# Kernel optimization log

Measured on AMD Instinct MI355X. Metric: run time of the kernel, lower is better.

Reference implementation:

```python
import jax, jax.numpy as jnp
import numpy as np

N = 8192
IN_F = 512
OUT_F = 256


def setup_inputs() -> dict:
    key = jax.random.key(0)
    k_x, k_adj, k_w, k_phi = jax.random.split(key, 4)
    x = jax.random.normal(k_x, (N, IN_F), dtype=jnp.float32)
    adj = jax.random.randint(k_adj, (N, N), 0, 2, dtype=jnp.int32)
    stdv_w = 1.0 / np.sqrt(OUT_F)
    weight = jax.random.uniform(k_w, (IN_F, OUT_F), minval=-stdv_w, maxval=stdv_w, dtype=jnp.float32)
    bias = jnp.zeros((OUT_F,), dtype=jnp.float32)
    stdv_p = 1.0  # 1/sqrt(phi.size(1)) = 1/sqrt(1)
    phi = jax.random.uniform(k_phi, (2 * OUT_F, 1), minval=-stdv_p, maxval=stdv_p, dtype=jnp.float32)
    return {"x": x, "adj": adj, "weight": weight, "bias": bias, "phi": phi}


def reference(x, adj, weight, bias, phi):
    # H = X W + b                                   [N, F]
    H = jnp.matmul(x, weight) + bias
    F_out = weight.shape[1]
    # Additive attention score: S[i,j] = [H_i ; H_j] . phi = H_i.phi_src + H_j.phi_dst
    # (H_interleaved indexes rows i, H_expanded indexes cols j in the torch code)
    s_src = jnp.matmul(H, phi[:F_out, 0])           # [N]
    s_dst = jnp.matmul(H, phi[F_out:, 0])           # [N]
    S = s_src[:, None] + s_dst[None, :]             # [N, N]
    n = x.shape[0]
    mask = (adj.astype(jnp.float32) + jnp.eye(n, dtype=jnp.float32)) != 0
    S_masked = jnp.where(mask, S, -jnp.inf)
    A = jax.nn.softmax(S_masked, axis=1)            # [N, N]
    return jnp.matmul(A, H)                         # [N, F]
```

## Files before the change

### kernel.cpp

```cpp
#include <hip/hip_runtime.h>
#include <hip/hip_bf16.h>
#include <stdint.h>

#define N_NODES 8192
#define IN_F 512
#define OUT_F 256
#define KSPLIT 4

typedef __attribute__((ext_vector_type(8))) short bf16x8;
typedef __attribute__((ext_vector_type(4))) float f32x4;

__device__ __forceinline__ unsigned short f2bf_rn(float f) {
  union { float f; unsigned u; } v; v.f = f;
  unsigned r = v.u + 0x7FFFu + ((v.u >> 16) & 1u);
  return (unsigned short)(r >> 16);
}
__device__ __forceinline__ float bf2f(unsigned short h) {
  union { unsigned u; float f; } v; v.u = ((unsigned)h) << 16;
  return v.f;
}

__device__ __forceinline__ void gload_lds16(const void* g, void* l) {
  __builtin_amdgcn_global_load_lds(
      (const __attribute__((address_space(1))) unsigned int*)g,
      (__attribute__((address_space(3))) unsigned int*)l, 16, 0, 0);
}

__device__ __forceinline__ bf16x8 expand8(uint2 b) {
  unsigned c0 = b.x, c1 = b.x >> 16, c2 = b.y, c3 = b.y >> 16;
  uint4 q;
  q.x = ((c0 & 1u) | ((c0 & 0x100u) << 8)) * 0x3F80u;
  q.y = ((c1 & 1u) | ((c1 & 0x100u) << 8)) * 0x3F80u;
  q.z = ((c2 & 1u) | ((c2 & 0x100u) << 8)) * 0x3F80u;
  q.w = ((c3 & 1u) | ((c3 & 0x100u) << 8)) * 0x3F80u;
  union { uint4 u; bf16x8 v; } r; r.u = q;
  return r.v;
}

__global__ __launch_bounds__(256) void k0_prep_w(const float* __restrict__ W,
                                                 short* __restrict__ Wh,
                                                 short* __restrict__ Wl) {
  int k = blockIdx.x;
  int c = threadIdx.x;
  float v = W[(size_t)k * OUT_F + c];
  unsigned short h = f2bf_rn(v);
  unsigned short l = f2bf_rn(v - bf2f(h));
  Wh[(size_t)c * IN_F + k] = (short)h;
  Wl[(size_t)c * IN_F + k] = (short)l;
}

__global__ __launch_bounds__(256) void k1_gemm_h(
    const float* __restrict__ X, const short* __restrict__ Wh,
    const short* __restrict__ Wl, const float* __restrict__ bias,
    float* __restrict__ H) {
  __shared__ __align__(16) short Xh[64 * 64], Xl[64 * 64];
  __shared__ __align__(16) short Wsh[128 * 64], Wsl[128 * 64];
  const int tid = threadIdx.x;
  const int rb = blockIdx.x >> 1, cb = blockIdx.x & 1;
  const int r0 = rb * 64, c0 = cb * 128;
  const int lane = tid & 63, wid = tid >> 6;

  f32x4 acc[8];
#pragma unroll
  for (int i = 0; i < 8; ++i) acc[i] = (f32x4){0.f, 0.f, 0.f, 0.f};

  const int sr = tid >> 2;
  const int sk = (tid & 3) * 16;

  for (int kc = 0; kc < IN_F; kc += 64) {
    const float* xp = X + (size_t)(r0 + sr) * IN_F + kc + sk;
#pragma unroll
    for (int q = 0; q < 2; ++q) {
      f32x4 v0 = *(const f32x4*)(xp + q * 8);
      f32x4 v1 = *(const f32x4*)(xp + q * 8 + 4);
      bf16x8 hv, lv;
#pragma unroll
      for (int j = 0; j < 4; ++j) {
        unsigned short h0 = f2bf_rn(v0[j]);
        hv[j] = (short)h0; lv[j] = (short)f2bf_rn(v0[j] - bf2f(h0));
        unsigned short h1 = f2bf_rn(v1[j]);
        hv[4 + j] = (short)h1; lv[4 + j] = (short)f2bf_rn(v1[j] - bf2f(h1));
      }
      int kb = (sk >> 3) + q;
      int off = sr * 64 + ((kb ^ (sr & 7)) << 3);
      *(bf16x8*)(Xh + off) = hv;
      *(bf16x8*)(Xl + off) = lv;
    }
#pragma unroll
    for (int it = 0; it < 4; ++it) {
      int u = it * 256 + tid;
      int col = u >> 3, kb = u & 7;
      size_t goff = (size_t)(c0 + col) * IN_F + kc + kb * 8;
      int off = col * 64 + ((kb ^ (col & 7)) << 3);
      *(bf16x8*)(Wsh + off) = *(const bf16x8*)(Wh + goff);
      *(bf16x8*)(Wsl + off) = *(const bf16x8*)(Wl + goff);
    }
    __syncthreads();
    const int arow = wid * 16 + (lane & 15);
    const int khalf = lane >> 4;
#pragma unroll
    for (int ks = 0; ks < 2; ++ks) {
      int kb = ks * 4 + khalf;
      int aoff = arow * 64 + ((kb ^ (arow & 7)) << 3);
      bf16x8 ah = *(const bf16x8*)(Xh + aoff);
      bf16x8 al = *(const bf16x8*)(Xl + aoff);
#pragma unroll
      for (int n = 0; n < 8; ++n) {
        int col = n * 16 + (lane & 15);
        int boff = col * 64 + ((kb ^ (col & 7)) << 3);
        bf16x8 bh = *(const bf16x8*)(Wsh + boff);
        bf16x8 bl = *(const bf16x8*)(Wsl + boff);
        acc[n] = __builtin_amdgcn_mfma_f32_16x16x32_bf16(ah, bh, acc[n], 0, 0, 0);
        acc[n] = __builtin_amdgcn_mfma_f32_16x16x32_bf16(ah, bl, acc[n], 0, 0, 0);
        acc[n] = __builtin_amdgcn_mfma_f32_16x16x32_bf16(al, bh, acc[n], 0, 0, 0);
      }
    }
    __syncthreads();
  }
  const int orow = r0 + wid * 16 + ((lane >> 4) << 2);
#pragma unroll
  for (int n = 0; n < 8; ++n) {
    int col = c0 + n * 16 + (lane & 15);
    float b = bias[col];
#pragma unroll
    for (int r = 0; r < 4; ++r)
      H[(size_t)(orow + r) * OUT_F + col] = acc[n][r] + b;
  }
}

__global__ __launch_bounds__(256) void k2_sdst(const float* __restrict__ H,
                                               const float* __restrict__ phi,
                                               float* __restrict__ sdst,
                                               float* __restrict__ blockmax) {
  __shared__ float r4[4];
  const int tid = threadIdx.x, lane = tid & 63, wid = tid >> 6;
  const int row = blockIdx.x * 4 + wid;
  f32x4 hv = *(const f32x4*)(H + (size_t)row * OUT_F + lane * 4);
  f32x4 pv = *(const f32x4*)(phi + OUT_F + lane * 4);
  float s = hv[0] * pv[0] + hv[1] * pv[1] + hv[2] * pv[2] + hv[3] * pv[3];
#pragma unroll
  for (int off = 32; off; off >>= 1) s += __shfl_xor(s, off);
  if (lane == 0) { sdst[row] = s; r4[wid] = s; }
  __syncthreads();
  if (tid == 0)
    blockmax[blockIdx.x] = fmaxf(fmaxf(r4[0], r4[1]), fmaxf(r4[2], r4[3]));
}

__global__ __launch_bounds__(256) void k4_build(const float* __restrict__ H,
                                                const float* __restrict__ sdst,
                                                const float* __restrict__ blockmax,
                                                short* __restrict__ Bs,
                                                float* __restrict__ e) {
  __shared__ float t[64][65];
  __shared__ float red[4];
  const int tid = threadIdx.x;
  float m = -1e30f;
  for (int i = tid; i < 2048; i += 256) m = fmaxf(m, blockmax[i]);
#pragma unroll
  for (int off = 32; off; off >>= 1) m = fmaxf(m, __shfl_xor(m, off));
  if ((tid & 63) == 0) red[tid >> 6] = m;
  __syncthreads();
  const float gmax = fmaxf(fmaxf(red[0], red[1]), fmaxf(red[2], red[3]));

  const int tx = tid & 63, ty = tid >> 6;
  const int j0 = (blockIdx.x >> 2) * 64;
  const int c0 = (blockIdx.x & 3) * 64;
#pragma unroll
  for (int i = 0; i < 16; ++i)
    t[ty + i * 4][tx] = H[(size_t)(j0 + ty + i * 4) * OUT_F + c0 + tx];
  __syncthreads();
  const float ej = expf(sdst[j0 + tx] - gmax);
#pragma unroll
  for (int i = 0; i < 16; ++i) {
    int c = c0 + ty + i * 4;
    float v = ej * t[tx][ty + i * 4];
    unsigned short h = f2bf_rn(v);
    unsigned short l = f2bf_rn(v - bf2f(h));
    size_t kidx = (size_t)j0 + (tx ^ ((c & 7) << 3));
    Bs[(size_t)c * N_NODES + kidx] = (short)h;
    Bs[(size_t)(256 + c) * N_NODES + kidx] = (short)l;
  }
  if (c0 == 0 && tid < 64) e[j0 + tid] = expf(sdst[j0 + tid] - gmax);
}

__global__ __launch_bounds__(512) void k5_main(
    const int* __restrict__ adj, const short* __restrict__ Bs,
    const float* __restrict__ e, float* __restrict__ part,
    float* __restrict__ dpartg, int kchunk) {
  __shared__ __align__(16) unsigned char Ab[2][128 * 64];
  __shared__ __align__(16) short Bb[2][2 * 256 * 64];

  const int tid = threadIdx.x;
  const int bid = (int)(blockIdx.x & 7) * 32 + (int)(blockIdx.x >> 3);
  const int rb = bid & 63, ksi = bid >> 6;
  const int r0 = rb * 128;
  const long kbeg = (long)ksi * kchunk;
  const int lane = tid & 63, wid = tid >> 6;
  const int wr = wid >> 2, wc = wid & 3;

  f32x4 acc[4][4];
#pragma unroll
  for (int mi = 0; mi < 4; ++mi)
#pragma unroll
    for (int ni = 0; ni < 4; ++ni) acc[mi][ni] = (f32x4){0.f, 0.f, 0.f, 0.f};

  const int sr = tid >> 2;
  const int skq = tid & 3;
  const int sk = skq * 16;
  const int irow = r0 + sr;
  float dsum = 0.f;

  int4 a0, a1, a2, a3;
  f32x4 ev0, ev1, ev2, ev3;

  auto issueA = [&](long kc) {
    const int* ap = adj + (size_t)irow * N_NODES + kc + sk;
    a0 = ((const int4*)ap)[0]; a1 = ((const int4*)ap)[1];
    a2 = ((const int4*)ap)[2]; a3 = ((const int4*)ap)[3];
    const float* ep = e + kc + sk;
    ev0 = ((const f32x4*)ep)[0]; ev1 = ((const f32x4*)ep)[1];
    ev2 = ((const f32x4*)ep)[2]; ev3 = ((const f32x4*)ep)[3];
  };
  auto issueB = [&](long kc, int buf) {
    const int p = wid >> 2;
    const int cg = wid & 3;
    const short* base = Bs + (size_t)p * 256 * N_NODES + kc;
#pragma unroll
    for (int i = 0; i < 8; ++i) {
      int col = cg * 64 + i * 8 + (lane >> 3);
      const short* g = base + (size_t)col * N_NODES + (lane & 7) * 8;
      short* l = &Bb[buf][(p * 256 + cg * 64 + i * 8) * 64];
      gload_lds16(g, l);
    }
  };
  auto finishA = [&](int buf) {
    dsum += (float)a0.x * ev0[0] + (float)a0.y * ev0[1] +
            (float)a0.z * ev0[2] + (float)a0.w * ev0[3];
    dsum += (float)a1.x * ev1[0] + (float)a1.y * ev1[1] +
            (float)a1.z * ev1[2] + (float)a1.w * ev1[3];
    dsum += (float)a2.x * ev2[0] + (float)a2.y * ev2[1] +
            (float)a2.z * ev2[2] + (float)a2.w * ev2[3];
    dsum += (float)a3.x * ev3[0] + (float)a3.y * ev3[1] +
            (float)a3.z * ev3[2] + (float)a3.w * ev3[3];
    unsigned u0 = (unsigned)a0.x | ((unsigned)a0.y << 8) |
                  ((unsigned)a0.z << 16) | ((unsigned)a0.w << 24);
    unsigned u1 = (unsigned)a1.x | ((unsigned)a1.y << 8) |
                  ((unsigned)a1.z << 16) | ((unsigned)a1.w << 24);
    unsigned u2 = (unsigned)a2.x | ((unsigned)a2.y << 8) |
                  ((unsigned)a2.z << 16) | ((unsigned)a2.w << 24);
    unsigned u3 = (unsigned)a3.x | ((unsigned)a3.y << 8) |
                  ((unsigned)a3.z << 16) | ((unsigned)a3.w << 24);
    const int g0 = skq * 2, g1 = g0 + 1;
    uint2 w0; w0.x = u0; w0.y = u1;
    uint2 w1; w1.x = u2; w1.y = u3;
    *(uint2*)&Ab[buf][sr * 64 + ((g0 ^ (sr & 7)) << 3)] = w0;
    *(uint2*)&Ab[buf][sr * 64 + ((g1 ^ (sr & 7)) << 3)] = w1;
  };
  auto compute = [&](int buf) {
#pragma unroll
    for (int ks = 0; ks < 2; ++ks) {
      const int kb = ks * 4 + (lane >> 4);
      bf16x8 af[4];
#pragma unroll
      for (int mi = 0; mi < 4; ++mi) {
        int row = wr * 64 + mi * 16 + (lane & 15);
        uint2 b = *(const uint2*)&Ab[buf][row * 64 + ((kb ^ (row & 7)) << 3)];
        af[mi] = expand8(b);
      }
#pragma unroll
      for (int ni = 0; ni < 4; ++ni) {
        int col = wc * 64 + ni * 16 + (lane & 15);
        int so = (kb ^ (col & 7)) << 3;
        bf16x8 bh = *(const bf16x8*)&Bb[buf][col * 64 + so];
        bf16x8 bl = *(const bf16x8*)&Bb[buf][(256 + col) * 64 + so];
#pragma unroll
        for (int mi = 0; mi < 4; ++mi) {
          acc[mi][ni] = __builtin_amdgcn_mfma_f32_16x16x32_bf16(af[mi], bh, acc[mi][ni], 0, 0, 0);
          acc[mi][ni] = __builtin_amdgcn_mfma_f32_16x16x32_bf16(af[mi], bl, acc[mi][ni], 0, 0, 0);
        }
      }
    }
  };

  issueA(kbeg); issueB(kbeg, 0); finishA(0);
  __syncthreads();

  const int NT = kchunk >> 6;
  for (int t = 0; t < NT; ++t) {
    const int cur = t & 1;
    if (t + 1 < NT) {
      const long kc = kbeg + (long)(t + 1) * 64;
      issueA(kc);
      issueB(kc, cur ^ 1);
    }
    compute(cur);
    if (t + 1 < NT) finishA(cur ^ 1);
    __syncthreads();
  }

  dsum += __shfl_xor(dsum, 1);
  dsum += __shfl_xor(dsum, 2);
  if ((tid & 3) == 0) dpartg[(size_t)ksi * N_NODES + irow] = dsum;

  float* pbase = part + (size_t)ksi * N_NODES * OUT_F;
  const int orow0 = r0 + wr * 64 + ((lane >> 4) << 2);
#pragma unroll
  for (int mi = 0; mi < 4; ++mi) {
    int orow = orow0 + mi * 16;
#pragma unroll
    for (int ni = 0; ni < 4; ++ni) {
      int col = wc * 64 + ni * 16 + (lane & 15);
#pragma unroll
      for (int r = 0; r < 4; ++r)
        pbase[(size_t)(orow + r) * OUT_F + col] = acc[mi][ni][r];
    }
  }
}

__global__ __launch_bounds__(256) void k6_final(const float* __restrict__ part,
                                                const float* __restrict__ dpart,
                                                const float* __restrict__ H,
                                                const float* __restrict__ e,
                                                const int* __restrict__ adj,
                                                float* __restrict__ out) {
  const int i = blockIdx.x, f = threadIdx.x;
  float num = 0.f, den = 0.f;
#pragma unroll
  for (int p = 0; p < KSPLIT; ++p) {
    num += part[((size_t)p * N_NODES + i) * OUT_F + f];
    den += dpart[(size_t)p * N_NODES + i];
  }
  if (adj[(size_t)i * N_NODES + i] == 0) {
    float ei = e[i];
    num += ei * H[(size_t)i * OUT_F + f];
    den += ei;
  }
  out[(size_t)i * OUT_F + f] = num / den;
}

extern "C" void kernel_launch(void* const* d_in, const int* in_sizes, int n_in,
                              void* d_out, int out_size, void* d_ws, size_t ws_size,
                              hipStream_t stream) {
  const float* x    = (const float*)d_in[0];
  const int*   adj  = (const int*)d_in[1];
  const float* w    = (const float*)d_in[2];
  const float* bias = (const float*)d_in[3];
  const float* phi  = (const float*)d_in[4];
  float* out = (float*)d_out;
  char* ws = (char*)d_ws;

  size_t off = 0;
  auto alloc = [&](size_t bytes) {
    size_t o = off; off += (bytes + 255) & ~(size_t)255; return o;
  };
  size_t oH   = alloc((size_t)N_NODES * OUT_F * 4);
  size_t oWh  = alloc((size_t)OUT_F * IN_F * 2);
  size_t oWl  = alloc((size_t)OUT_F * IN_F * 2);
  size_t oSd  = alloc((size_t)N_NODES * 4);
  size_t oBm  = alloc((size_t)2048 * 4);
  size_t oE   = alloc((size_t)N_NODES * 4);
  size_t oBs  = alloc((size_t)2 * OUT_F * N_NODES * 2);
  size_t oPart = alloc((size_t)KSPLIT * N_NODES * OUT_F * 4);
  size_t oDp   = alloc((size_t)KSPLIT * N_NODES * 4);
  (void)oDp; (void)ws_size;

  float* H   = (float*)(ws + oH);
  short* Wh  = (short*)(ws + oWh);
  short* Wl  = (short*)(ws + oWl);
  float* Sd  = (float*)(ws + oSd);
  float* Bm  = (float*)(ws + oBm);
  float* E   = (float*)(ws + oE);
  short* Bs  = (short*)(ws + oBs);
  float* Part = (float*)(ws + oPart);
  float* Dp   = (float*)(ws + oDp);

  k0_prep_w<<<IN_F, OUT_F, 0, stream>>>(w, Wh, Wl);
  k1_gemm_h<<<256, 256, 0, stream>>>(x, Wh, Wl, bias, H);
  k2_sdst<<<N_NODES / 4, 256, 0, stream>>>(H, phi, Sd, Bm);
  k4_build<<<512, 256, 0, stream>>>(H, Sd, Bm, Bs, E);
  k5_main<<<64 * KSPLIT, 512, 0, stream>>>(adj, Bs, E, Part, Dp, N_NODES / KSPLIT);
  k6_final<<<N_NODES, 256, 0, stream>>>(Part, Dp, H, E, adj, out);
}
```

Before: 483.0 us.

## Pack adjacency into transposed bitmask in a separate kernel; split main GEMM by columns

Adds a pre-pass kernel that reads the int32 adjacency once, folds in the self-loop, ballots it into 64-bit transposed bitmasks and computes the softmax denominator per row. The main MFMA kernel now reads compact bitmask words instead of re-reading int32 adjacency, and it is split into 512 blocks of 256 threads, each covering half of the output columns, which doubles the block count. The final kernel is simplified to divide by the precomputed denominator, and the workspace is reordered so the H/W buffers alias the partial-sum buffer. This trades an extra kernel launch and a bitmask write for much less adjacency traffic inside the GEMM and more parallelism, though B tiles are now loaded twice across column halves.

```diff
diff --git a/kernel.cpp b/kernel.cpp
--- a/kernel.cpp
+++ b/kernel.cpp
@@ -26,14 +26,12 @@
       (__attribute__((address_space(3))) unsigned int*)l, 16, 0, 0);
 }
 
-__device__ __forceinline__ bf16x8 expand8(uint2 b) {
-  unsigned c0 = b.x, c1 = b.x >> 16, c2 = b.y, c3 = b.y >> 16;
-  uint4 q;
-  q.x = ((c0 & 1u) | ((c0 & 0x100u) << 8)) * 0x3F80u;
-  q.y = ((c1 & 1u) | ((c1 & 0x100u) << 8)) * 0x3F80u;
-  q.z = ((c2 & 1u) | ((c2 & 0x100u) << 8)) * 0x3F80u;
-  q.w = ((c3 & 1u) | ((c3 & 0x100u) << 8)) * 0x3F80u;
-  union { uint4 u; bf16x8 v; } r; r.u = q;
+__device__ __forceinline__ bf16x8 expand_byte(unsigned m) {
+  union { uint4 u; bf16x8 v; } r;
+  r.u.x = ((m & 1u) | ((m & 2u) << 15)) * 0x3F80u;
+  r.u.y = (((m >> 2) & 1u) | (((m >> 3) & 1u) << 16)) * 0x3F80u;
+  r.u.z = (((m >> 4) & 1u) | (((m >> 5) & 1u) << 16)) * 0x3F80u;
+  r.u.w = (((m >> 6) & 1u) | (((m >> 7) & 1u) << 16)) * 0x3F80u;
   return r.v;
 }
 
@@ -183,20 +181,45 @@
   if (c0 == 0 && tid < 64) e[j0 + tid] = expf(sdst[j0 + tid] - gmax);
 }
 
-__global__ __launch_bounds__(512) void k5_main(
-    const int* __restrict__ adj, const short* __restrict__ Bs,
-    const float* __restrict__ e, float* __restrict__ part,
-    float* __restrict__ dpartg, int kchunk) {
-  __shared__ __align__(16) unsigned char Ab[2][128 * 64];
-  __shared__ __align__(16) short Bb[2][2 * 256 * 64];
+__global__ __launch_bounds__(512) void k3_bits(const int* __restrict__ adj,
+                                               const float* __restrict__ e,
+                                               unsigned long long* __restrict__ bitsT,
+                                               float* __restrict__ denom) {
+  const int tid = threadIdx.x, lane = tid & 63, wid = tid >> 6;
+  const int row = blockIdx.x * 8 + wid;
+  const int* ap = adj + (size_t)row * N_NODES;
+  float ds = 0.f;
+#pragma unroll 2
+  for (int w = 0; w < 128; ++w) {
+    int col = w * 64 + lane;
+    int v = ap[col];
+    bool m = (v != 0) || (col == row);
+    unsigned long long word = __ballot(m);
+    ds += m ? e[col] : 0.f;
+    if (lane == 0) bitsT[(size_t)w * N_NODES + row] = word;
+  }
+#pragma unroll
+  for (int off = 32; off; off >>= 1) ds += __shfl_xor(ds, off);
+  if (lane == 0) denom[row] = ds;
+}
+
+__global__ __launch_bounds__(256) void k5_main(
+    const unsigned long long* __restrict__ bitsT,
+    const short* __restrict__ Bs,
+    float* __restrict__ part, int kchunk) {
+  __shared__ __align__(16) unsigned long long Abits[2][128];
+  __shared__ __align__(16) short Bb[2][2 * 128 * 64];
 
   const int tid = threadIdx.x;
-  const int bid = (int)(blockIdx.x & 7) * 32 + (int)(blockIdx.x >> 3);
-  const int rb = bid & 63, ksi = bid >> 6;
-  const int r0 = rb * 128;
+  const int orig = (int)blockIdx.x;
+  const int rb = orig >> 3;
+  const int x = orig & 7;
+  const int cb = x & 1, ksi = x >> 1;
+  const int r0 = rb * 128, c0 = cb * 128;
+  const int w0 = ksi * 32;
   const long kbeg = (long)ksi * kchunk;
   const int lane = tid & 63, wid = tid >> 6;
-  const int wr = wid >> 2, wc = wid & 3;
+  const int wr = wid >> 1, wc = wid & 1;
 
   f32x4 acc[4][4];
 #pragma unroll
@@ -204,75 +227,45 @@
 #pragma unroll
     for (int ni = 0; ni < 4; ++ni) acc[mi][ni] = (f32x4){0.f, 0.f, 0.f, 0.f};
 
-  const int sr = tid >> 2;
-  const int skq = tid & 3;
-  const int sk = skq * 16;
-  const int irow = r0 + sr;
-  float dsum = 0.f;
-
-  int4 a0, a1, a2, a3;
-  f32x4 ev0, ev1, ev2, ev3;
-
-  auto issueA = [&](long kc) {
-    const int* ap = adj + (size_t)irow * N_NODES + kc + sk;
-    a0 = ((const int4*)ap)[0]; a1 = ((const int4*)ap)[1];
-    a2 = ((const int4*)ap)[2]; a3 = ((const int4*)ap)[3];
-    const float* ep = e + kc + sk;
-    ev0 = ((const f32x4*)ep)[0]; ev1 = ((const f32x4*)ep)[1];
-    ev2 = ((const f32x4*)ep)[2]; ev3 = ((const f32x4*)ep)[3];
+  auto stage = [&](int t, int buf) {
+    if (wid == 0)
+      gload_lds16(bitsT + (size_t)(w0 + t) * N_NODES + r0 + lane * 2,
+                  &Abits[buf][lane * 2]);
+    const long kc = kbeg + (long)t * 64;
+    const int p = wid >> 1, cg = wid & 1;
+    const short* base = Bs + (size_t)p * 256 * N_NODES + kc;
+#pragma unroll
+    for (int i = 0; i < 8; ++i) {
+      int col = c0 + cg * 64 + i * 8 + (lane >> 3);
+      const short* g = base + (size_t)col * N_NODES + (lane & 7) * 8;
+      short* l = &Bb[buf][(p * 128 + cg * 64 + i * 8) * 64];
+      gload_lds16(g, l);
+    }
   };
-  auto issueB = [&](long kc, int buf) {
-    const int p = wid >> 2;
-    const int cg = wid & 3;
-    const short* base = Bs + (size_t)p * 256 * N_NODES + kc;
-#pragma unroll
-    for (int i = 0; i < 8; ++i) {
-      int col = cg * 64 + i * 8 + (lane >> 3);
-      const short* g = base + (size_t)col * N_NODES + (lane & 7) * 8;
-      short* l = &Bb[buf][(p * 256 + cg * 64 + i * 8) * 64];
-      gload_lds16(g, l);
-    }
-  };
-  auto finishA = [&](int buf) {
-    dsum += (float)a0.x * ev0[0] + (float)a0.y * ev0[1] +
-            (float)a0.z * ev0[2] + (float)a0.w * ev0[3];
-    dsum += (float)a1.x * ev1[0] + (float)a1.y * ev1[1] +
-            (float)a1.z * ev1[2] + (float)a1.w * ev1[3];
-    dsum += (float)a2.x * ev2[0] + (float)a2.y * ev2[1] +
-            (float)a2.z * ev2[2] + (float)a2.w * ev2[3];
-    dsum += (float)a3.x * ev3[0] + (float)a3.y * ev3[1] +
-            (float)a3.z * ev3[2] + (float)a3.w * ev3[3];
-    unsigned u0 = (unsigned)a0.x | ((unsigned)a0.y << 8) |
-                  ((unsigned)a0.z << 16) | ((unsigned)a0.w << 24);
-    unsigned u1 = (unsigned)a1.x | ((unsigned)a1.y << 8) |
-                  ((unsigned)a1.z << 16) | ((unsigned)a1.w << 24);
-    unsigned u2 = (unsigned)a2.x | ((unsigned)a2.y << 8) |
-                  ((unsigned)a2.z << 16) | ((unsigned)a2.w << 24);
-    unsigned u3 = (unsigned)a3.x | ((unsigned)a3.y << 8) |
-                  ((unsigned)a3.z << 16) | ((unsigned)a3.w << 24);
-    const int g0 = skq * 2, g1 = g0 + 1;
-    uint2 w0; w0.x = u0; w0.y = u1;
-    uint2 w1; w1.x = u2; w1.y = u3;
-    *(uint2*)&Ab[buf][sr * 64 + ((g0 ^ (sr & 7)) << 3)] = w0;
-    *(uint2*)&Ab[buf][sr * 64 + ((g1 ^ (sr & 7)) << 3)] = w1;
-  };
+
   auto compute = [&](int buf) {
+    uint2 aw[4];
+#pragma unroll
+    for (int mi = 0; mi < 4; ++mi) {
+      int row = wr * 64 + mi * 16 + (lane & 15);
+      aw[mi] = *(const uint2*)&Abits[buf][row];
+    }
+    const int bsh = (lane >> 4) * 8;
 #pragma unroll
     for (int ks = 0; ks < 2; ++ks) {
       const int kb = ks * 4 + (lane >> 4);
       bf16x8 af[4];
 #pragma unroll
       for (int mi = 0; mi < 4; ++mi) {
-        int row = wr * 64 + mi * 16 + (lane & 15);
-        uint2 b = *(const uint2*)&Ab[buf][row * 64 + ((kb ^ (row & 7)) << 3)];
-        af[mi] = expand8(b);
+        unsigned m = ((ks ? aw[mi].y : aw[mi].x) >> bsh) & 0xFFu;
+        af[mi] = expand_byte(m);
       }
 #pragma unroll
       for (int ni = 0; ni < 4; ++ni) {
-        int col = wc * 64 + ni * 16 + (lane & 15);
-        int so = (kb ^ (col & 7)) << 3;
-        bf16x8 bh = *(const bf16x8*)&Bb[buf][col * 64 + so];
-        bf16x8 bl = *(const bf16x8*)&Bb[buf][(256 + col) * 64 + so];
+        int colL = wc * 64 + ni * 16 + (lane & 15);
+        int so = (kb ^ (colL & 7)) << 3;
+        bf16x8 bh = *(const bf16x8*)&Bb[buf][colL * 64 + so];
+        bf16x8 bl = *(const bf16x8*)&Bb[buf][(128 + colL) * 64 + so];
 #pragma unroll
         for (int mi = 0; mi < 4; ++mi) {
           acc[mi][ni] = __builtin_amdgcn_mfma_f32_16x16x32_bf16(af[mi], bh, acc[mi][ni], 0, 0, 0);
@@ -282,25 +275,15 @@
     }
   };
 
-  issueA(kbeg); issueB(kbeg, 0); finishA(0);
+  stage(0, 0);
   __syncthreads();
-
   const int NT = kchunk >> 6;
   for (int t = 0; t < NT; ++t) {
     const int cur = t & 1;
-    if (t + 1 < NT) {
-      const long kc = kbeg + (long)(t + 1) * 64;
-      issueA(kc);
-      issueB(kc, cur ^ 1);
-    }
+    if (t + 1 < NT) stage(t + 1, cur ^ 1);
     compute(cur);
-    if (t + 1 < NT) finishA(cur ^ 1);
     __syncthreads();
   }
-
-  dsum += __shfl_xor(dsum, 1);
-  dsum += __shfl_xor(dsum, 2);
-  if ((tid & 3) == 0) dpartg[(size_t)ksi * N_NODES + irow] = dsum;
 
   float* pbase = part + (size_t)ksi * N_NODES * OUT_F;
   const int orow0 = r0 + wr * 64 + ((lane >> 4) << 2);
@@ -309,7 +292,7 @@
     int orow = orow0 + mi * 16;
 #pragma unroll
     for (int ni = 0; ni < 4; ++ni) {
-      int col = wc * 64 + ni * 16 + (lane & 15);
+      int col = c0 + wc * 64 + ni * 16 + (lane & 15);
 #pragma unroll
       for (int r = 0; r < 4; ++r)
         pbase[(size_t)(orow + r) * OUT_F + col] = acc[mi][ni][r];
@@ -318,24 +301,14 @@
 }
 
 __global__ __launch_bounds__(256) void k6_final(const float* __restrict__ part,
-                                                const float* __restrict__ dpart,
-                                                const float* __restrict__ H,
-                                                const float* __restrict__ e,
-                                                const int* __restrict__ adj,
+                                                const float* __restrict__ denom,
                                                 float* __restrict__ out) {
   const int i = blockIdx.x, f = threadIdx.x;
-  float num = 0.f, den = 0.f;
-#pragma unroll
-  for (int p = 0; p < KSPLIT; ++p) {
+  float num = 0.f;
+#pragma unroll
+  for (int p = 0; p < KSPLIT; ++p)
     num += part[((size_t)p * N_NODES + i) * OUT_F + f];
-    den += dpart[(size_t)p * N_NODES + i];
-  }
-  if (adj[(size_t)i * N_NODES + i] == 0) {
-    float ei = e[i];
-    num += ei * H[(size_t)i * OUT_F + f];
-    den += ei;
-  }
-  out[(size_t)i * OUT_F + f] = num / den;
+  out[(size_t)i * OUT_F + f] = num / denom[i];
 }
 
 extern "C" void kernel_launch(void* const* d_in, const int* in_sizes, int n_in,
@@ -349,20 +322,22 @@
   float* out = (float*)d_out;
   char* ws = (char*)d_ws;
 
+  const size_t PART_BYTES = (size_t)KSPLIT * N_NODES * OUT_F * 4;
   size_t off = 0;
   auto alloc = [&](size_t bytes) {
     size_t o = off; off += (bytes + 255) & ~(size_t)255; return o;
   };
-  size_t oH   = alloc((size_t)N_NODES * OUT_F * 4);
-  size_t oWh  = alloc((size_t)OUT_F * IN_F * 2);
-  size_t oWl  = alloc((size_t)OUT_F * IN_F * 2);
-  size_t oSd  = alloc((size_t)N_NODES * 4);
-  size_t oBm  = alloc((size_t)2048 * 4);
+  size_t oPart = alloc(PART_BYTES);
+  size_t oH  = 0;
+  size_t oWh = oH + (size_t)N_NODES * OUT_F * 4;
+  size_t oWl = oWh + (size_t)OUT_F * IN_F * 2;
+  size_t oSd = oWl + (size_t)OUT_F * IN_F * 2;
+  size_t oBm = oSd + (size_t)N_NODES * 4;
   size_t oE   = alloc((size_t)N_NODES * 4);
   size_t oBs  = alloc((size_t)2 * OUT_F * N_NODES * 2);
-  size_t oPart = alloc((size_t)KSPLIT * N_NODES * OUT_F * 4);
-  size_t oDp   = alloc((size_t)KSPLIT * N_NODES * 4);
-  (void)oDp; (void)ws_size;
+  size_t oBit = alloc((size_t)128 * N_NODES * 8);
+  size_t oDen = alloc((size_t)N_NODES * 4);
+  (void)ws_size;
 
   float* H   = (float*)(ws + oH);
   short* Wh  = (short*)(ws + oWh);
@@ -371,13 +346,15 @@
   float* Bm  = (float*)(ws + oBm);
   float* E   = (float*)(ws + oE);
   short* Bs  = (short*)(ws + oBs);
+  unsigned long long* Bits = (unsigned long long*)(ws + oBit);
+  float* Den = (float*)(ws + oDen);
   float* Part = (float*)(ws + oPart);
-  float* Dp   = (float*)(ws + oDp);
 
   k0_prep_w<<<IN_F, OUT_F, 0, stream>>>(w, Wh, Wl);
   k1_gemm_h<<<256, 256, 0, stream>>>(x, Wh, Wl, bias, H);
   k2_sdst<<<N_NODES / 4, 256, 0, stream>>>(H, phi, Sd, Bm);
   k4_build<<<512, 256, 0, stream>>>(H, Sd, Bm, Bs, E);
-  k5_main<<<64 * KSPLIT, 512, 0, stream>>>(adj, Bs, E, Part, Dp, N_NODES / KSPLIT);
-  k6_final<<<N_NODES, 256, 0, stream>>>(Part, Dp, H, E, adj, out);
-}
+  k3_bits<<<N_NODES / 8, 512, 0, stream>>>(adj, E, Bits, Den);
+  k5_main<<<512, 256, 0, stream>>>(Bits, Bs, Part, N_NODES / KSPLIT);
+  k6_final<<<N_NODES, 256, 0, stream>>>(Part, Den, out);
+}
```

After: 549.7 us. 13.8% more time.
